# Kernel optimization log

Measured on AMD Instinct MI355X. Metric: run time of the kernel, lower is better.

## Reference

```python
import jax, jax.numpy as jnp
import numpy as np

N_NODES = 100000
N_EDGES = 1600000
HIDDEN = 64
EMB = 2
N_GRAPHS = 64


def gcn_conv(x, W, b, src, dst, ew, n_nodes):
    # PyG GCNConv: add self-loops (weight 1), symmetric normalization,
    # transform-then-propagate, messages flow src -> dst.
    loop = jnp.arange(n_nodes, dtype=src.dtype)
    s = jnp.concatenate([src, loop])
    d = jnp.concatenate([dst, loop])
    w = jnp.concatenate([ew, jnp.ones((n_nodes,), dtype=ew.dtype)])
    deg = jax.ops.segment_sum(w, d, num_segments=n_nodes)  # [N]
    dinv = jnp.where(deg > 0, jax.lax.rsqrt(deg), 0.0)
    norm = dinv[s] * w * dinv[d]                            # [E+N]
    h = x @ W                                               # [N, out]
    msg = h[s] * norm[:, None]                              # [E+N, out]
    out = jax.ops.segment_sum(msg, d, num_segments=n_nodes)
    return out + b


def batch_norm(x, gamma, beta, eps=1e-5):
    mu = jnp.mean(x, axis=0)
    var = jnp.var(x, axis=0)
    return (x - mu) * jax.lax.rsqrt(var + eps) * gamma + beta


def global_mean_pool(x, batch, n_graphs):
    s = jax.ops.segment_sum(x, batch, num_segments=n_graphs)
    cnt = jax.ops.segment_sum(jnp.ones((x.shape[0],), x.dtype), batch, num_segments=n_graphs)
    return s / jnp.maximum(cnt, 1.0)[:, None]


def setup_inputs() -> dict:
    key = jax.random.key(0)
    ks = jax.random.split(key, 8)
    x = jax.random.normal(ks[0], (N_NODES, 1), dtype=jnp.float32)
    edge_index = jax.random.randint(ks[1], (2, N_EDGES), 0, N_NODES, dtype=jnp.int32)
    edge_weight = jax.random.uniform(ks[2], (N_EDGES,), dtype=jnp.float32)
    batch = jnp.sort(jax.random.randint(ks[3], (N_NODES,), 0, N_GRAPHS, dtype=jnp.int32))
    W1 = jax.random.normal(ks[4], (1, HIDDEN), dtype=jnp.float32) * (1.0 / np.sqrt(1))
    b1 = jnp.zeros((HIDDEN,), jnp.float32)
    gamma = jnp.ones((HIDDEN,), jnp.float32)
    beta = jnp.zeros((HIDDEN,), jnp.float32)
    W2 = jax.random.normal(ks[5], (HIDDEN, EMB), dtype=jnp.float32) * (1.0 / np.sqrt(HIDDEN))
    b2 = jnp.zeros((EMB,), jnp.float32)
    return {"x": x, "edge_index": edge_index, "edge_weight": edge_weight, "batch": batch,
            "W1": W1, "b1": b1, "gamma": gamma, "beta": beta, "W2": W2, "b2": b2}


def reference(x, edge_index, edge_weight, batch, W1, b1, gamma, beta, W2, b2):
    src, dst = edge_index[0], edge_index[1]
    h = gcn_conv(x, W1, b1, src, dst, edge_weight, N_NODES)
    h = batch_norm(h, gamma, beta)
    h = jax.nn.relu(h)
    # eval mode: dropout / adj_dropout are identity
    h = gcn_conv(h, W2, b2, src, dst, edge_weight, N_NODES)
    return global_mean_pool(h, batch, N_GRAPHS)
```

## Files before the change

kernel.cpp:

```cpp
#include <hip/hip_runtime.h>

#define NN 100000
#define NE 1600000
#define NH 64
#define NG 64

#define RSH 9
#define RNG 512
#define RB  196
#define CAP 16384
#define BB  256

static constexpr int TPB = 256;

__global__ __launch_bounds__(1024) void k_scatter_dyn(const int* __restrict__ src,
                                                      const int* __restrict__ dst,
                                                      const float* __restrict__ w,
                                                      int* __restrict__ cur,
                                                      uint2* __restrict__ ebuf) {
    __shared__ int cl[RB];
    __shared__ int lcur[RB];
    const int b = blockIdx.x, tid = threadIdx.x;
    for (int i = tid; i < RB; i += 1024) cl[i] = 0;
    __syncthreads();
    long e0 = ((long)b * NE / BB) & ~3L;
    long e1 = (b == BB - 1) ? NE : (((long)(b + 1) * NE / BB) & ~3L);
    for (long e = e0 + (long)tid * 4; e < e1; e += 4096L) {
        int4 d4 = *reinterpret_cast<const int4*>(dst + e);
        atomicAdd(&cl[d4.x >> RSH], 1);
        atomicAdd(&cl[d4.y >> RSH], 1);
        atomicAdd(&cl[d4.z >> RSH], 1);
        atomicAdd(&cl[d4.w >> RSH], 1);
    }
    __syncthreads();
    for (int i = tid; i < RB; i += 1024) lcur[i] = atomicAdd(&cur[i], cl[i]);
    __syncthreads();
    for (long e = e0 + (long)tid * 4; e < e1; e += 4096L) {
        int4 d4 = *reinterpret_cast<const int4*>(dst + e);
        int4 s4 = *reinterpret_cast<const int4*>(src + e);
        float4 w4 = *reinterpret_cast<const float4*>(w + e);
        int dd[4] = {d4.x, d4.y, d4.z, d4.w};
        int ss[4] = {s4.x, s4.y, s4.z, s4.w};
        float wv[4] = {w4.x, w4.y, w4.z, w4.w};
#pragma unroll
        for (int k = 0; k < 4; ++k) {
            int r = dd[k] >> RSH;
            int slot = atomicAdd(&lcur[r], 1);
            if (slot < CAP) {
                unsigned pack = ((unsigned)(dd[k] & (RNG - 1)) << 17) | (unsigned)ss[k];
                ebuf[(size_t)r * CAP + slot] = make_uint2(pack, __float_as_uint(wv[k]));
            }
        }
    }
}

__global__ __launch_bounds__(1024) void kB_deg(const uint2* __restrict__ ebuf,
                                               const int* __restrict__ cur,
                                               const float* __restrict__ x,
                                               const int* __restrict__ batch,
                                               float* __restrict__ dinv,
                                               float* __restrict__ g1,
                                               float* __restrict__ cnt) {
    __shared__ float bins[RNG];
    __shared__ int hist[NG];
    const int r = blockIdx.x, tid = threadIdx.x;
    if (tid < RNG) bins[tid] = 0.f;
    if (tid >= RNG && tid < RNG + NG) hist[tid - RNG] = 0;
    __syncthreads();
    int nr = min(cur[r], CAP);
    const uint2* eb = ebuf + (size_t)r * CAP;
    for (int i = tid; i < nr; i += 1024) {
        uint2 ed = eb[i];
        atomicAdd(&bins[ed.x >> 17], __uint_as_float(ed.y));
    }
    __syncthreads();
    int base = r * RNG;
    int len = min(RNG, NN - base);
    if (tid < len) {
        int n = base + tid;
        float di = rsqrtf(bins[tid] + 1.0f);
        dinv[n] = di;
        g1[n] = di * x[n];
        atomicAdd(&hist[batch[n]], 1);
    }
    __syncthreads();
    if (tid < NG && hist[tid] > 0) atomicAdd(&cnt[tid], (float)hist[tid]);
}

__global__ __launch_bounds__(1024) void kB_t1(const uint2* __restrict__ ebuf,
                                              const int* __restrict__ cur,
                                              const float* __restrict__ g1,
                                              const float* __restrict__ dinv,
                                              float* __restrict__ agg1,
                                              float* __restrict__ scal) {
    __shared__ float bins[RNG];
    const int r = blockIdx.x, tid = threadIdx.x;
    if (tid < RNG) bins[tid] = 0.f;
    __syncthreads();
    int nr = min(cur[r], CAP);
    const uint2* eb = ebuf + (size_t)r * CAP;
    for (int i = tid; i < nr; i += 1024) {
        uint2 ed = eb[i];
        atomicAdd(&bins[ed.x >> 17], __uint_as_float(ed.y) * g1[ed.x & 0x1FFFF]);
    }
    __syncthreads();
    int base = r * RNG;
    int len = min(RNG, NN - base);
    float a = 0.f;
    if (tid < len) {
        int n = base + tid;
        a = dinv[n] * (bins[tid] + g1[n]);
        agg1[n] = a;
    }
    float sm = a, q = a * a;
    for (int off = 32; off > 0; off >>= 1) {
        sm += __shfl_down(sm, off);
        q  += __shfl_down(q, off);
    }
    __shared__ float red[2][16];
    int wave = tid >> 6, lane = tid & 63;
    if (lane == 0) { red[0][wave] = sm; red[1][wave] = q; }
    __syncthreads();
    if (tid == 0) {
        float ss = 0.f, qq = 0.f;
        for (int i = 0; i < 16; ++i) { ss += red[0][i]; qq += red[1][i]; }
        atomicAdd(&scal[0], ss);
        atomicAdd(&scal[1], qq);
    }
}

__global__ void k_node_hp(const float* __restrict__ agg1, const float* __restrict__ dinv,
                          const float* __restrict__ scal, const float* __restrict__ W1,
                          const float* __restrict__ gamma, const float* __restrict__ beta,
                          const float* __restrict__ W2, float* __restrict__ g2) {
    __shared__ float tabs[4 * NH];
    float mu = scal[0] * (1.0f / NN);
    if (threadIdx.x < NH) {
        int j = threadIdx.x;
        float var = scal[1] * (1.0f / NN) - mu * mu;
        float w1 = W1[j];
        tabs[j]          = w1 * gamma[j] * rsqrtf(var * w1 * w1 + 1e-5f);
        tabs[NH + j]     = beta[j];
        tabs[2 * NH + j] = W2[2 * j];
        tabs[3 * NH + j] = W2[2 * j + 1];
    }
    __syncthreads();
    int n = blockIdx.x * blockDim.x + threadIdx.x;
    if (n < NN) {
        float av = agg1[n] - mu;
        float h0 = 0.f, h1 = 0.f;
#pragma unroll
        for (int j = 0; j < NH; ++j) {
            float t = fmaxf(fmaf(av, tabs[j], tabs[NH + j]), 0.f);
            h0 = fmaf(t, tabs[2 * NH + j], h0);
            h1 = fmaf(t, tabs[3 * NH + j], h1);
        }
        float di = dinv[n];
        g2[2 * n] = di * h0; g2[2 * n + 1] = di * h1;
    }
}

__global__ __launch_bounds__(1024) void kB_t2_fin(const uint2* __restrict__ ebuf,
                                                  const int* __restrict__ cur,
                                                  const float* __restrict__ g2,
                                                  const float* __restrict__ dinv,
                                                  const int* __restrict__ batch,
                                                  float* __restrict__ pooled,
                                                  float* __restrict__ cnt,
                                                  const float* __restrict__ b2,
                                                  int* __restrict__ done,
                                                  float* __restrict__ out) {
    __shared__ float2 bins2[RNG];
    __shared__ float pl[NG][2];
    __shared__ int winner;
    const int r = blockIdx.x, tid = threadIdx.x;
    if (tid < RNG) bins2[tid] = make_float2(0.f, 0.f);
    if (tid >= RNG && tid < RNG + 2 * NG) ((float*)pl)[tid - RNG] = 0.f;
    __syncthreads();
    int nr = min(cur[r], CAP);
    const uint2* eb = ebuf + (size_t)r * CAP;
    for (int i = tid; i < nr; i += 1024) {
        uint2 ed = eb[i];
        int sidx = ed.x & 0x1FFFF;
        float ww = __uint_as_float(ed.y);
        float2 g = *reinterpret_cast<const float2*>(g2 + 2 * sidx);
        int off = ed.x >> 17;
        atomicAdd(&bins2[off].x, ww * g.x);
        atomicAdd(&bins2[off].y, ww * g.y);
    }
    __syncthreads();
    int base = r * RNG;
    int len = min(RNG, NN - base);
    if (tid < len) {
        int n = base + tid;
        float di = dinv[n];
        float a0 = di * (bins2[tid].x + g2[2 * n]);
        float a1 = di * (bins2[tid].y + g2[2 * n + 1]);
        int g = batch[n];
        atomicAdd(&pl[g][0], a0);
        atomicAdd(&pl[g][1], a1);
    }
    __syncthreads();
    if (tid < NG) {
        float p0 = pl[tid][0], p1 = pl[tid][1];
        if (p0 != 0.f || p1 != 0.f) {
            atomicAdd(&pooled[2 * tid],     p0);
            atomicAdd(&pooled[2 * tid + 1], p1);
        }
    }
    __syncthreads();
    if (tid == 0) {
        int t = __hip_atomic_fetch_add(done, 1, __ATOMIC_ACQ_REL, __HIP_MEMORY_SCOPE_AGENT);
        winner = (t == gridDim.x - 1) ? 1 : 0;
        if (winner) __builtin_amdgcn_fence(__ATOMIC_ACQUIRE, "agent");
    }
    __syncthreads();
    if (winner && tid < 2 * NG) {
        float pv = __hip_atomic_load(&pooled[tid], __ATOMIC_RELAXED, __HIP_MEMORY_SCOPE_AGENT);
        float cg = __hip_atomic_load(&cnt[tid >> 1], __ATOMIC_RELAXED, __HIP_MEMORY_SCOPE_AGENT);
        out[tid] = pv / fmaxf(cg, 1.0f) + (cg > 0.f ? b2[tid & 1] : 0.f);
    }
}


__global__ void k_edge_deg_fb(const int* __restrict__ dst, const float* __restrict__ w,
                              float* __restrict__ deg) {
    int gid = blockIdx.x * blockDim.x + threadIdx.x;
    int T = gridDim.x * blockDim.x;
    for (int e = gid; e < NE; e += T) atomicAdd(&deg[dst[e]], w[e]);
}

__global__ void k_node_dinv_fb(const float* __restrict__ x, float* __restrict__ deg,
                               float* __restrict__ agg1, float* __restrict__ scal) {
    int gid = blockIdx.x * blockDim.x + threadIdx.x;
    int T = gridDim.x * blockDim.x;
    for (int n = gid; n < NN; n += T) {
        float di = rsqrtf(deg[n] + 1.0f);
        deg[n] = di;
        agg1[n] = di * di * x[n];
    }
    if (gid == 0) { scal[0] = 0.f; scal[1] = 0.f; }
}

__global__ void k_edge_agg1_fb(const int* __restrict__ src, const int* __restrict__ dst,
                               const float* __restrict__ w, const float* __restrict__ dinv,
                               const float* __restrict__ x, float* __restrict__ agg1) {
    int gid = blockIdx.x * blockDim.x + threadIdx.x;
    int T = gridDim.x * blockDim.x;
    for (int e = gid; e < NE; e += T) {
        int s = src[e], d = dst[e];
        atomicAdd(&agg1[d], dinv[s] * w[e] * dinv[d] * x[s]);
    }
}

__global__ void k_reduce_fb(const float* __restrict__ agg1, float* __restrict__ scal) {
    float s = 0.f, q = 0.f;
    int gid = blockIdx.x * blockDim.x + threadIdx.x;
    int T = gridDim.x * blockDim.x;
    for (int n = gid; n < NN; n += T) { float a = agg1[n]; s += a; q += a * a; }
    for (int off = 32; off > 0; off >>= 1) { s += __shfl_down(s, off); q += __shfl_down(q, off); }
    __shared__ float red[2][4];
    int wave = threadIdx.x >> 6, lane = threadIdx.x & 63;
    if (lane == 0) { red[0][wave] = s; red[1][wave] = q; }
    __syncthreads();
    if (threadIdx.x == 0) {
        atomicAdd(&scal[0], red[0][0] + red[0][1] + red[0][2] + red[0][3]);
        atomicAdd(&scal[1], red[1][0] + red[1][1] + red[1][2] + red[1][3]);
    }
}

__global__ void k_prep_fb(float* __restrict__ scal, const float* __restrict__ W1,
                          const float* __restrict__ gamma, float* __restrict__ c,
                          float* __restrict__ pooled, float* __restrict__ cnt) {
    int j = threadIdx.x;
    float mu  = scal[0] * (1.0f / NN);
    float var = scal[1] * (1.0f / NN) - mu * mu;
    float w1 = W1[j];
    c[j] = w1 * gamma[j] * rsqrtf(var * w1 * w1 + 1e-5f);
    pooled[2 * j] = 0.f; pooled[2 * j + 1] = 0.f; cnt[j] = 0.f;
    if (j == 0) scal[2] = mu;
}

__global__ void k_node_hp_fb(const float* __restrict__ agg1, const float* __restrict__ dinv,
                             const float* __restrict__ c, const float* __restrict__ beta,
                             const float* __restrict__ W2, const float* __restrict__ scal,
                             float* __restrict__ hp, float* __restrict__ agg2) {
    __shared__ float sc[NH], sb[NH], s0[NH], s1[NH];
    if (threadIdx.x < NH) {
        int j = threadIdx.x;
        sc[j] = c[j]; sb[j] = beta[j]; s0[j] = W2[2 * j]; s1[j] = W2[2 * j + 1];
    }
    __syncthreads();
    float mu = scal[2];
    int n = blockIdx.x * blockDim.x + threadIdx.x;
    if (n < NN) {
        float a = agg1[n] - mu;
        float h0 = 0.f, h1 = 0.f;
#pragma unroll
        for (int j = 0; j < NH; ++j) {
            float t = fmaxf(fmaf(a, sc[j], sb[j]), 0.f);
            h0 = fmaf(t, s0[j], h0);
            h1 = fmaf(t, s1[j], h1);
        }
        hp[2 * n] = h0; hp[2 * n + 1] = h1;
        float sl = dinv[n] * dinv[n];
        agg2[2 * n] = sl * h0; agg2[2 * n + 1] = sl * h1;
    }
}

__global__ void k_edge_agg2_fb(const int* __restrict__ src, const int* __restrict__ dst,
                               const float* __restrict__ w, const float* __restrict__ dinv,
                               const float* __restrict__ hp, float* __restrict__ agg2) {
    int gid = blockIdx.x * blockDim.x + threadIdx.x;
    int T = gridDim.x * blockDim.x;
    for (int e = gid; e < NE; e += T) {
        int s = src[e], d = dst[e];
        float nrm = dinv[s] * w[e] * dinv[d];
        float2 h = *reinterpret_cast<const float2*>(hp + 2 * s);
        atomicAdd(&agg2[2 * d],     nrm * h.x);
        atomicAdd(&agg2[2 * d + 1], nrm * h.y);
    }
}

__global__ void k_pool_fb(const float* __restrict__ agg2, const int* __restrict__ batch,
                          float* __restrict__ pooled, float* __restrict__ cnt) {
    __shared__ float ls0[NG], ls1[NG], lc[NG];
    if (threadIdx.x < NG) { ls0[threadIdx.x] = 0.f; ls1[threadIdx.x] = 0.f; lc[threadIdx.x] = 0.f; }
    __syncthreads();
    int gid = blockIdx.x * blockDim.x + threadIdx.x;
    int T = gridDim.x * blockDim.x;
    for (int n = gid; n < NN; n += T) {
        int b = batch[n];
        float2 v = *reinterpret_cast<const float2*>(agg2 + 2 * n);
        atomicAdd(&ls0[b], v.x); atomicAdd(&ls1[b], v.y); atomicAdd(&lc[b], 1.f);
    }
    __syncthreads();
    if (threadIdx.x < NG) {
        int g = threadIdx.x;
        atomicAdd(&pooled[2 * g], ls0[g]);
        atomicAdd(&pooled[2 * g + 1], ls1[g]);
        atomicAdd(&cnt[g], lc[g]);
    }
}

__global__ void k_final_fb(const float* __restrict__ pooled, const float* __restrict__ cnt,
                           const float* __restrict__ b2, float* __restrict__ out) {
    int i = threadIdx.x;
    if (i < 2 * NG) {
        int g = i >> 1, k = i & 1;
        float cg = cnt[g];
        out[i] = pooled[i] / fmaxf(cg, 1.0f) + (cg > 0.f ? b2[k] : 0.f);
    }
}

extern "C" void kernel_launch(void* const* d_in, const int* in_sizes, int n_in,
                              void* d_out, int out_size, void* d_ws, size_t ws_size,
                              hipStream_t stream) {
    const float* x     = (const float*)d_in[0];
    const int*   ei    = (const int*)  d_in[1];
    const float* ew    = (const float*)d_in[2];
    const int*   batch = (const int*)  d_in[3];
    const float* W1    = (const float*)d_in[4];
    const float* gamma = (const float*)d_in[6];
    const float* beta  = (const float*)d_in[7];
    const float* W2    = (const float*)d_in[8];
    const float* b2    = (const float*)d_in[9];
    float* out = (float*)d_out;

    float* ws = (float*)d_ws;
    float* dinv   = ws;
    float* g1     = ws + NN;
    float* agg1   = ws + 2 * NN;
    float* hp     = ws + 3 * NN;
    float* g2     = ws + 5 * NN;
    float* agg2   = ws + 7 * NN;
    float* scal   = ws + 9 * NN;
    float* cbuf   = ws + 9 * NN + 16;
    float* pooled = ws + 9 * NN + 80;
    float* cnt    = ws + 9 * NN + 208;
    int*   meta   = (int*)(ws + 9 * NN + 272);
    uint2* ebuf   = (uint2*)(ws + 9 * NN + 272 + 256);

    int* cur  = meta;
    int* done = meta + 200;

    const int* srcp = ei;
    const int* dstp = ei + NE;

    size_t availF = ws_size / sizeof(float);
    size_t needF  = 9 * (size_t)NN + 272 + 256 + 2 * (size_t)RB * CAP + 64;

    const int NB = (NN + TPB - 1) / TPB;

    if (availF >= needF) {
        hipMemsetAsync(ws + 9 * NN, 0, (272 + 256) * sizeof(float), stream);
        k_scatter_dyn<<<BB, 1024, 0, stream>>>(srcp, dstp, ew, cur, ebuf);
        kB_deg       <<<RB, 1024, 0, stream>>>(ebuf, cur, x, batch, dinv, g1, cnt);
        kB_t1        <<<RB, 1024, 0, stream>>>(ebuf, cur, g1, dinv, agg1, scal);
        k_node_hp    <<<NB, TPB, 0, stream>>>(agg1, dinv, scal, W1, gamma, beta, W2, g2);
        kB_t2_fin    <<<RB, 1024, 0, stream>>>(ebuf, cur, g2, dinv, batch, pooled, cnt, b2, done, out);
    } else {
        const int ebl = 2048;
        hipMemsetAsync(dinv, 0, NN * sizeof(float), stream);
        k_edge_deg_fb <<<ebl, TPB, 0, stream>>>(dstp, ew, dinv);
        k_node_dinv_fb<<<NB, TPB, 0, stream>>>(x, dinv, agg1, scal);
        k_edge_agg1_fb<<<ebl, TPB, 0, stream>>>(srcp, dstp, ew, dinv, x, agg1);
        k_reduce_fb   <<<256, TPB, 0, stream>>>(agg1, scal);
        k_prep_fb     <<<1, 64, 0, stream>>>(scal, W1, gamma, cbuf, pooled, cnt);
        k_node_hp_fb  <<<NB, TPB, 0, stream>>>(agg1, dinv, cbuf, beta, W2, scal, hp, agg2);
        k_edge_agg2_fb<<<ebl, TPB, 0, stream>>>(srcp, dstp, ew, dinv, hp, agg2);
        k_pool_fb     <<<128, TPB, 0, stream>>>(agg2, batch, pooled, cnt);
        k_final_fb    <<<1, 128, 0, stream>>>(pooled, cnt, b2, out);
    }
}
```

Baseline: 91.25 us.

## Use per-block private edge buckets instead of global atomic bucket cursors

The scatter kernel now writes edges into a private fixed-capacity slot region per (block, destination range), so it no longer needs a counting pass over dst or global atomics to reserve space. Per-block counts are published to a count table that the consumer kernels read. Zeroing of the small accumulators moves into block 0 of the scatter kernel, which drops the memset launch. In exchange, the consumers loop over all padded slots with a division and bounds check, and any bucket that overflows its capacity of 80 silently drops edges.

Measured after the change: 86.24 us. 5.5% less time.

```diff
diff --git a/kernel.cpp b/kernel.cpp
--- a/kernel.cpp
+++ b/kernel.cpp
@@ -8,33 +8,32 @@
 #define RSH 9
 #define RNG 512
 #define RB  196
-#define CAP 16384
 #define BB  256
+#define CAPB 80
 
 static constexpr int TPB = 256;
 
-__global__ __launch_bounds__(1024) void k_scatter_dyn(const int* __restrict__ src,
-                                                      const int* __restrict__ dst,
-                                                      const float* __restrict__ w,
-                                                      int* __restrict__ cur,
-                                                      uint2* __restrict__ ebuf) {
-    __shared__ int cl[RB];
+__global__ __launch_bounds__(1024) void k_scatter1(const int* __restrict__ src,
+                                                   const int* __restrict__ dst,
+                                                   const float* __restrict__ w,
+                                                   int* __restrict__ cnts,
+                                                   float* __restrict__ scal,
+                                                   float* __restrict__ pooled,
+                                                   float* __restrict__ cnt,
+                                                   int* __restrict__ done,
+                                                   uint2* __restrict__ ebuf) {
     __shared__ int lcur[RB];
     const int b = blockIdx.x, tid = threadIdx.x;
-    for (int i = tid; i < RB; i += 1024) cl[i] = 0;
+    if (b == 0) {
+        if (tid < 2) scal[tid] = 0.f;
+        if (tid >= 64 && tid < 192) pooled[tid - 64] = 0.f;
+        if (tid >= 192 && tid < 256) cnt[tid - 192] = 0.f;
+        if (tid == 256) *done = 0;
+    }
+    for (int i = tid; i < RB; i += 1024) lcur[i] = 0;
     __syncthreads();
     long e0 = ((long)b * NE / BB) & ~3L;
     long e1 = (b == BB - 1) ? NE : (((long)(b + 1) * NE / BB) & ~3L);
-    for (long e = e0 + (long)tid * 4; e < e1; e += 4096L) {
-        int4 d4 = *reinterpret_cast<const int4*>(dst + e);
-        atomicAdd(&cl[d4.x >> RSH], 1);
-        atomicAdd(&cl[d4.y >> RSH], 1);
-        atomicAdd(&cl[d4.z >> RSH], 1);
-        atomicAdd(&cl[d4.w >> RSH], 1);
-    }
-    __syncthreads();
-    for (int i = tid; i < RB; i += 1024) lcur[i] = atomicAdd(&cur[i], cl[i]);
-    __syncthreads();
     for (long e = e0 + (long)tid * 4; e < e1; e += 4096L) {
         int4 d4 = *reinterpret_cast<const int4*>(dst + e);
         int4 s4 = *reinterpret_cast<const int4*>(src + e);
@@ -46,32 +45,38 @@
         for (int k = 0; k < 4; ++k) {
             int r = dd[k] >> RSH;
             int slot = atomicAdd(&lcur[r], 1);
-            if (slot < CAP) {
+            if (slot < CAPB) {
                 unsigned pack = ((unsigned)(dd[k] & (RNG - 1)) << 17) | (unsigned)ss[k];
-                ebuf[(size_t)r * CAP + slot] = make_uint2(pack, __float_as_uint(wv[k]));
+                ebuf[((size_t)b * RB + r) * CAPB + slot] = make_uint2(pack, __float_as_uint(wv[k]));
             }
         }
     }
+    __syncthreads();
+    for (int i = tid; i < RB; i += 1024) cnts[i * BB + b] = min(lcur[i], CAPB);
 }
 
 __global__ __launch_bounds__(1024) void kB_deg(const uint2* __restrict__ ebuf,
-                                               const int* __restrict__ cur,
+                                               const int* __restrict__ cnts,
                                                const float* __restrict__ x,
                                                const int* __restrict__ batch,
                                                float* __restrict__ dinv,
                                                float* __restrict__ g1,
                                                float* __restrict__ cnt) {
     __shared__ float bins[RNG];
+    __shared__ int scnt[BB];
     __shared__ int hist[NG];
     const int r = blockIdx.x, tid = threadIdx.x;
     if (tid < RNG) bins[tid] = 0.f;
+    if (tid < BB) scnt[tid] = cnts[r * BB + tid];
     if (tid >= RNG && tid < RNG + NG) hist[tid - RNG] = 0;
     __syncthreads();
-    int nr = min(cur[r], CAP);
-    const uint2* eb = ebuf + (size_t)r * CAP;
-    for (int i = tid; i < nr; i += 1024) {
-        uint2 ed = eb[i];
-        atomicAdd(&bins[ed.x >> 17], __uint_as_float(ed.y));
+    const uint2* ebr = ebuf + (size_t)r * CAPB;
+    for (int i = tid; i < BB * CAPB; i += 1024) {
+        int b = i / CAPB, j = i - b * CAPB;
+        if (j < scnt[b]) {
+            uint2 ed = ebr[(size_t)b * (RB * CAPB) + j];
+            atomicAdd(&bins[ed.x >> 17], __uint_as_float(ed.y));
+        }
     }
     __syncthreads();
     int base = r * RNG;
@@ -88,20 +93,24 @@
 }
 
 __global__ __launch_bounds__(1024) void kB_t1(const uint2* __restrict__ ebuf,
-                                              const int* __restrict__ cur,
+                                              const int* __restrict__ cnts,
                                               const float* __restrict__ g1,
                                               const float* __restrict__ dinv,
                                               float* __restrict__ agg1,
                                               float* __restrict__ scal) {
     __shared__ float bins[RNG];
+    __shared__ int scnt[BB];
     const int r = blockIdx.x, tid = threadIdx.x;
     if (tid < RNG) bins[tid] = 0.f;
-    __syncthreads();
-    int nr = min(cur[r], CAP);
-    const uint2* eb = ebuf + (size_t)r * CAP;
-    for (int i = tid; i < nr; i += 1024) {
-        uint2 ed = eb[i];
-        atomicAdd(&bins[ed.x >> 17], __uint_as_float(ed.y) * g1[ed.x & 0x1FFFF]);
+    if (tid < BB) scnt[tid] = cnts[r * BB + tid];
+    __syncthreads();
+    const uint2* ebr = ebuf + (size_t)r * CAPB;
+    for (int i = tid; i < BB * CAPB; i += 1024) {
+        int b = i / CAPB, j = i - b * CAPB;
+        if (j < scnt[b]) {
+            uint2 ed = ebr[(size_t)b * (RB * CAPB) + j];
+            atomicAdd(&bins[ed.x >> 17], __uint_as_float(ed.y) * g1[ed.x & 0x1FFFF]);
+        }
     }
     __syncthreads();
     int base = r * RNG;
@@ -161,7 +170,7 @@
 }
 
 __global__ __launch_bounds__(1024) void kB_t2_fin(const uint2* __restrict__ ebuf,
-                                                  const int* __restrict__ cur,
+                                                  const int* __restrict__ cnts,
                                                   const float* __restrict__ g2,
                                                   const float* __restrict__ dinv,
                                                   const int* __restrict__ batch,
@@ -171,22 +180,26 @@
                                                   int* __restrict__ done,
                                                   float* __restrict__ out) {
     __shared__ float2 bins2[RNG];
+    __shared__ int scnt[BB];
     __shared__ float pl[NG][2];
     __shared__ int winner;
     const int r = blockIdx.x, tid = threadIdx.x;
     if (tid < RNG) bins2[tid] = make_float2(0.f, 0.f);
+    if (tid < BB) scnt[tid] = cnts[r * BB + tid];
     if (tid >= RNG && tid < RNG + 2 * NG) ((float*)pl)[tid - RNG] = 0.f;
     __syncthreads();
-    int nr = min(cur[r], CAP);
-    const uint2* eb = ebuf + (size_t)r * CAP;
-    for (int i = tid; i < nr; i += 1024) {
-        uint2 ed = eb[i];
-        int sidx = ed.x & 0x1FFFF;
-        float ww = __uint_as_float(ed.y);
-        float2 g = *reinterpret_cast<const float2*>(g2 + 2 * sidx);
-        int off = ed.x >> 17;
-        atomicAdd(&bins2[off].x, ww * g.x);
-        atomicAdd(&bins2[off].y, ww * g.y);
+    const uint2* ebr = ebuf + (size_t)r * CAPB;
+    for (int i = tid; i < BB * CAPB; i += 1024) {
+        int b = i / CAPB, j = i - b * CAPB;
+        if (j < scnt[b]) {
+            uint2 ed = ebr[(size_t)b * (RB * CAPB) + j];
+            int sidx = ed.x & 0x1FFFF;
+            float ww = __uint_as_float(ed.y);
+            float2 g = *reinterpret_cast<const float2*>(g2 + 2 * sidx);
+            int off = ed.x >> 17;
+            atomicAdd(&bins2[off].x, ww * g.x);
+            atomicAdd(&bins2[off].y, ww * g.y);
+        }
     }
     __syncthreads();
     int base = r * RNG;
@@ -378,27 +391,24 @@
     float* cbuf   = ws + 9 * NN + 16;
     float* pooled = ws + 9 * NN + 80;
     float* cnt    = ws + 9 * NN + 208;
-    int*   meta   = (int*)(ws + 9 * NN + 272);
-    uint2* ebuf   = (uint2*)(ws + 9 * NN + 272 + 256);
-
-    int* cur  = meta;
-    int* done = meta + 200;
+    int*   cnts   = (int*)(ws + 9 * NN + 272);
+    int*   done   = cnts + RB * BB;
+    uint2* ebuf   = (uint2*)(ws + 9 * NN + 272 + 50184);
 
     const int* srcp = ei;
     const int* dstp = ei + NE;
 
     size_t availF = ws_size / sizeof(float);
-    size_t needF  = 9 * (size_t)NN + 272 + 256 + 2 * (size_t)RB * CAP + 64;
+    size_t needF  = 9 * (size_t)NN + 272 + 50184 + 2 * (size_t)BB * RB * CAPB + 64;
 
     const int NB = (NN + TPB - 1) / TPB;
 
     if (availF >= needF) {
-        hipMemsetAsync(ws + 9 * NN, 0, (272 + 256) * sizeof(float), stream);
-        k_scatter_dyn<<<BB, 1024, 0, stream>>>(srcp, dstp, ew, cur, ebuf);
-        kB_deg       <<<RB, 1024, 0, stream>>>(ebuf, cur, x, batch, dinv, g1, cnt);
-        kB_t1        <<<RB, 1024, 0, stream>>>(ebuf, cur, g1, dinv, agg1, scal);
-        k_node_hp    <<<NB, TPB, 0, stream>>>(agg1, dinv, scal, W1, gamma, beta, W2, g2);
-        kB_t2_fin    <<<RB, 1024, 0, stream>>>(ebuf, cur, g2, dinv, batch, pooled, cnt, b2, done, out);
+        k_scatter1<<<BB, 1024, 0, stream>>>(srcp, dstp, ew, cnts, scal, pooled, cnt, done, ebuf);
+        kB_deg    <<<RB, 1024, 0, stream>>>(ebuf, cnts, x, batch, dinv, g1, cnt);
+        kB_t1     <<<RB, 1024, 0, stream>>>(ebuf, cnts, g1, dinv, agg1, scal);
+        k_node_hp <<<NB, TPB, 0, stream>>>(agg1, dinv, scal, W1, gamma, beta, W2, g2);
+        kB_t2_fin <<<RB, 1024, 0, stream>>>(ebuf, cnts, g2, dinv, batch, pooled, cnt, b2, done, out);
     } else {
         const int ebl = 2048;
         hipMemsetAsync(dinv, 0, NN * sizeof(float), stream);
```
